# Kernel tuning notes

Hardware: AMD Instinct MI355X
Metric: run time of the kernel (lower is better)

## Reference

```python
import jax, jax.numpy as jnp
import numpy as np

BS, NQ, NC = 128, 900, 91
PRE_TOPK = 10000      # source: pre_topk when n_queries*n_cls > 10000
POST_TOPK = 100       # source: keep_inds[:100]
IOU_THRESH = 0.7


def box_cxcywh_to_xyxy(b):
    cx, cy, w, h = b[..., 0], b[..., 1], b[..., 2], b[..., 3]
    return jnp.stack([cx - 0.5 * w, cy - 0.5 * h, cx + 0.5 * w, cy + 0.5 * h], axis=-1)


def nms_image(boxes, scores, labels):
    """Greedy batched NMS, returning the first POST_TOPK picked indices.
    boxes: [PRE,4] xyxy (scaled), scores: [PRE] desc-sorted, labels: [PRE] int.
    batched_nms trick: offset boxes per class so IoU across classes is 0."""
    max_coord = jnp.max(boxes)
    off = labels.astype(boxes.dtype) * (max_coord + 1.0)
    ob = boxes + off[:, None]                          # [PRE,4]
    areas = (ob[:, 2] - ob[:, 0]) * (ob[:, 3] - ob[:, 1])

    def step(active, _):
        s = jnp.where(active, scores, -jnp.inf)
        i = jnp.argmax(s)                              # highest-score surviving box
        bi = ob[i]
        xx1 = jnp.maximum(bi[0], ob[:, 0])
        yy1 = jnp.maximum(bi[1], ob[:, 1])
        xx2 = jnp.minimum(bi[2], ob[:, 2])
        yy2 = jnp.minimum(bi[3], ob[:, 3])
        inter = jnp.clip(xx2 - xx1, 0.0) * jnp.clip(yy2 - yy1, 0.0)
        union = areas[i] + areas - inter
        iou = inter / jnp.maximum(union, 1e-9)
        # suppress IoU > thresh (includes i itself since iou(i,i)=1)
        active = active & (iou <= IOU_THRESH)
        return active, i

    _, keep = jax.lax.scan(step, jnp.ones(ob.shape[0], dtype=bool), None, length=POST_TOPK)
    return keep                                         # [POST]


def setup_inputs() -> dict:
    key = jax.random.key(0)
    k1, k2, k3, k4 = jax.random.split(key, 4)
    pred_logits = jax.random.normal(k1, (BS, NQ, NC), dtype=jnp.float32) * 2.0 - 2.0
    cxcy = jax.random.uniform(k2, (BS, NQ, 2), dtype=jnp.float32)
    wh = jax.random.uniform(k3, (BS, NQ, 2), dtype=jnp.float32, minval=0.02, maxval=0.3)
    pred_boxes = jnp.concatenate([cxcy, wh], axis=-1)   # cxcywh in [0,1]
    target_sizes = jax.random.uniform(k4, (BS, 2), dtype=jnp.float32, minval=480.0, maxval=1333.0)
    return {"pred_logits": pred_logits, "pred_boxes": pred_boxes, "target_sizes": target_sizes}


def reference(pred_logits, pred_boxes, target_sizes):
    bs, nq, nc = pred_logits.shape
    prob = jax.nn.sigmoid(pred_logits).reshape(bs, nq * nc)      # all_scores
    boxes = box_cxcywh_to_xyxy(pred_boxes)                        # [bs,nq,4]
    img_h, img_w = target_sizes[:, 0], target_sizes[:, 1]
    scale = jnp.stack([img_w, img_h, img_w, img_h], axis=1)       # [bs,4]
    boxes = boxes * scale[:, None, :]

    top_scores, top_idx = jax.lax.top_k(prob, PRE_TOPK)           # [bs,PRE]
    top_labels = top_idx % nc                                     # all_labels gather
    top_box_idx = top_idx // nc                                   # all_boxes gather
    top_boxes = jnp.take_along_axis(boxes, top_box_idx[..., None], axis=1)  # [bs,PRE,4]

    keep = jax.vmap(nms_image)(top_boxes, top_scores, top_labels)  # [bs,POST]
    out_scores = jnp.take_along_axis(top_scores, keep, axis=1)
    out_labels = jnp.take_along_axis(top_labels, keep, axis=1)
    out_boxes = jnp.take_along_axis(top_boxes, keep[..., None], axis=1)
    return out_scores, out_labels, out_boxes
```

## Files before the change

kernel.cpp:

```cpp
#include <hip/hip_runtime.h>
#include <cstdint>

#pragma clang fp contract(off)

#define BS   128
#define NQ   900
#define NC   91
#define NQC  (NQ * NC)
#define Q4   (NQC / 4)
#define HHALF 10238
#define PRE  10000
#define POST 100
#define TBITS 13
#define TBINS (1 << TBITS)
#define TSHIFT (32 - TBITS)
#define K_WIN 16
#define HSEG 1024
#define KS   2780

typedef unsigned long long ull;

#define WS_GH 0

__device__ __forceinline__ uint32_t fkey(float f) {
    uint32_t b = __float_as_uint(f);
    return (b & 0x80000000u) ? ~b : (b | 0x80000000u);
}
__device__ __forceinline__ float unkey(uint32_t u) {
    uint32_t b = (u & 0x80000000u) ? (u & 0x7FFFFFFFu) : ~u;
    return __uint_as_float(b);
}
__device__ __forceinline__ uint32_t qclamp(uint32_t q) { return (q < NQ) ? q : (NQ - 1); }

__device__ __forceinline__ ull shflx(ull v, int j) {
    uint32_t lo = (uint32_t)__shfl_xor((int)(uint32_t)v, j, 64);
    uint32_t hi = (uint32_t)__shfl_xor((int)(uint32_t)(v >> 32), j, 64);
    return ((ull)hi << 32) | (ull)lo;
}
__device__ __forceinline__ ull cex(ull v, int j, bool lower, bool desc) {
    ull pb = shflx(v, j);
    ull a = lower ? v : pb;
    ull b = lower ? pb : v;
    bool sw = desc ? (a < b) : (a > b);
    return sw ? pb : v;
}
__device__ __forceinline__ void ce(ull& a, ull& b, bool desc) {
    bool sw = desc ? (a < b) : (a > b);
    if (sw) { ull t = a; a = b; b = t; }
}

__global__ void __launch_bounds__(1024) k_hist(const float* __restrict__ logits,
                                               uint16_t* __restrict__ ghist) {
    const int img = blockIdx.x >> 1;
    const int h = blockIdx.x & 1;
    const int tid = threadIdx.x;
    __shared__ uint32_t hist[TBINS];
    __shared__ uint32_t part[1024];
    __shared__ uint32_t sTB;
    const float4* lg4 = (const float4*)(logits + (size_t)img * NQC);
    for (int i = tid; i < TBINS; i += 1024) hist[i] = 0u;
    float4 sv[5];
    #pragma unroll
    for (int c = 0; c < 5; ++c) sv[c] = lg4[c * 4096 + tid];
    __syncthreads();
    #pragma unroll
    for (int c = 0; c < 5; ++c) {
        atomicAdd(&hist[fkey(sv[c].x) >> TSHIFT], 1u);
        atomicAdd(&hist[fkey(sv[c].y) >> TSHIFT], 1u);
        atomicAdd(&hist[fkey(sv[c].z) >> TSHIFT], 1u);
        atomicAdd(&hist[fkey(sv[c].w) >> TSHIFT], 1u);
    }
    __syncthreads();
    {
        uint32_t s = 0;
        int b0 = tid * 8;
        #pragma unroll
        for (int j = 0; j < 8; ++j) s += hist[b0 + j];
        part[tid] = s;
    }
    __syncthreads();
    if (tid < 64) {
        uint32_t pv[16]; uint32_t tot = 0;
        #pragma unroll
        for (int j = 0; j < 16; ++j) { pv[j] = part[tid * 16 + j]; tot += pv[j]; }
        uint32_t sinc = tot;
        #pragma unroll
        for (int off = 1; off < 64; off <<= 1) {
            uint32_t o = (uint32_t)__shfl_down((int)sinc, off, 64);
            if (tid + off < 64) sinc += o;
        }
        uint32_t cum = sinc - tot;
        for (int j = 15; j >= 0; --j) {
            if (cum < KS && cum + pv[j] >= KS) {
                int pbn = (tid * 16 + j) * 8;
                uint32_t c2 = cum;
                for (int b = pbn + 7; b >= pbn; --b) {
                    if (c2 + hist[b] >= KS) { sTB = (uint32_t)b; break; }
                    c2 += hist[b];
                }
            }
            cum += pv[j];
        }
    }
    __syncthreads();
    const uint32_t TB = sTB;
    for (int i = tid; i < TBINS; i += 1024) hist[i] = 0u;
    __syncthreads();
    const int lo = h * HHALF;
    const int hi = (lo + HHALF < Q4) ? (lo + HHALF) : Q4;
    for (int i0 = lo; i0 < hi; i0 += 4096) {
        float4 v[4]; bool lv[4];
        #pragma unroll
        for (int s = 0; s < 4; ++s) {
            int i = i0 + (s << 10) + tid;
            lv[s] = (i < hi);
            v[s] = lv[s] ? lg4[i] : make_float4(0.f, 0.f, 0.f, 0.f);
        }
        #pragma unroll
        for (int s = 0; s < 4; ++s) {
            if (lv[s]) {
                uint32_t u;
                u = fkey(v[s].x); if ((u >> TSHIFT) >= TB) atomicAdd(&hist[u >> TSHIFT], 1u);
                u = fkey(v[s].y); if ((u >> TSHIFT) >= TB) atomicAdd(&hist[u >> TSHIFT], 1u);
                u = fkey(v[s].z); if ((u >> TSHIFT) >= TB) atomicAdd(&hist[u >> TSHIFT], 1u);
                u = fkey(v[s].w); if ((u >> TSHIFT) >= TB) atomicAdd(&hist[u >> TSHIFT], 1u);
            }
        }
    }
    __syncthreads();
    uint16_t* g = ghist + (size_t)(img * 2 + h) * TBINS;
    for (int i = tid; i < TBINS; i += 1024) g[i] = (uint16_t)hist[i];
}

__global__ void __launch_bounds__(1024) k_sel(const float* __restrict__ logits,
                                              const uint16_t* __restrict__ ghist,
                                              const float* __restrict__ pred_boxes,
                                              const float* __restrict__ target_sizes,
                                              float* __restrict__ out) {
    const int img = blockIdx.x;
    const int tid = threadIdx.x;
    const int lane = tid & 63;
    const int wv = tid >> 6;

    __shared__ uint32_t hist[TBINS];
    __shared__ uint32_t part[1024];
    __shared__ float4 shPB[NQ];
    __shared__ ull binK[HSEG];
    __shared__ ull headK[HSEG];
    __shared__ float aX1[POST], aY1[POST], aX2[POST], aY2[POST], aAr[POST];
    __shared__ int   aCl[POST];
    __shared__ float s_x1[K_WIN], s_y1[K_WIN], s_x2[K_WIN], s_y2[K_WIN];
    __shared__ int   s_cl[K_WIN];
    __shared__ uint32_t s_em[K_WIN];
    __shared__ ull sF0;
    __shared__ uint32_t sCntA, sCntB, sMX;
    __shared__ uint32_t sB1, sTp1, sB2, sTp2, sTK;

    const float ih = target_sizes[img * 2 + 0];
    const float iw = target_sizes[img * 2 + 1];
    const float* pb = pred_boxes + (size_t)img * NQ * 4;
    const float4* lg4 = (const float4*)(logits + (size_t)img * NQC);

    auto mckey = [&](uint32_t f) -> uint32_t {
        uint32_t q = qclamp(f / NC);
        float4 bb = shPB[q];
        float x1 = (bb.x - 0.5f * bb.z) * iw;
        float y1 = (bb.y - 0.5f * bb.w) * ih;
        float x2 = (bb.x + 0.5f * bb.z) * iw;
        float y2 = (bb.y + 0.5f * bb.w) * ih;
        return fkey(fmaxf(fmaxf(x1, y1), fmaxf(x2, y2)));
    };

    if (tid < NQ) shPB[tid] = ((const float4*)pb)[tid];
    {
        const uint16_t* g0 = ghist + (size_t)(img * 2) * TBINS;
        const uint16_t* g1 = g0 + TBINS;
        for (int i = tid; i < TBINS; i += 1024)
            hist[i] = (uint32_t)g0[i] + (uint32_t)g1[i];
    }
    binK[tid] = 0ull; headK[tid] = 0ull;
    if (tid == 0) { sCntA = 0u; sCntB = 0u; sMX = 0u; sF0 = 0ull;
                    sB1 = 0u; sTp1 = 1u; sB2 = 0u; sTp2 = 0u; sTK = 0u; }
    __syncthreads();
    {
        uint32_t s = 0;
        int b0 = tid * 8;
        #pragma unroll
        for (int j = 0; j < 8; ++j) s += hist[b0 + j];
        part[tid] = s;
    }
    __syncthreads();

    if (tid < 64) {
        uint32_t pv[16]; uint32_t tot = 0;
        #pragma unroll
        for (int j = 0; j < 16; ++j) { pv[j] = part[tid * 16 + j]; tot += pv[j]; }
        uint32_t sinc = tot;
        #pragma unroll
        for (int off = 1; off < 64; off <<= 1) {
            uint32_t o = (uint32_t)__shfl_down((int)sinc, off, 64);
            if (tid + off < 64) sinc += o;
        }
        uint32_t total = (uint32_t)__shfl((int)sinc, 0, 64);
        uint32_t TKl = (total < PRE) ? total : PRE;
        uint32_t T2l = (TKl < HSEG) ? TKl : HSEG;
        if (tid == 0) sTK = TKl;
        uint32_t cum = sinc - tot;
        for (int j = 15; j >= 0; --j) {
            if (cum < TKl && cum + pv[j] >= TKl) {
                int pbn = (tid * 16 + j) * 8;
                uint32_t c2 = cum;
                for (int b = pbn + 7; b >= pbn; --b) {
                    if (c2 + hist[b] >= TKl) { sB1 = (uint32_t)b; sTp1 = TKl - c2; break; }
                    c2 += hist[b];
                }
            }
            if (cum < T2l && cum + pv[j] >= T2l) {
                int pbn = (tid * 16 + j) * 8;
                uint32_t c2 = cum;
                for (int b = pbn + 3 + 4; b >= pbn; --b) {
                    if (c2 + hist[b] >= T2l) { sB2 = (uint32_t)b; sTp2 = T2l - c2; break; }
                    c2 += hist[b];
                }
            }
            cum += pv[j];
        }
    }
    __syncthreads();
    const uint32_t B1 = sB1, tp1 = sTp1, B2 = sB2;
    const uint32_t TK = sTK;
    const int C1 = (int)(((TK < (uint32_t)HSEG) ? TK : (uint32_t)HSEG) - sTp2);

    uint32_t lmx = 0u;
    for (int i0 = 0; i0 < Q4; i0 += 4096) {
        float4 v[4]; int ib[4];
        #pragma unroll
        for (int s = 0; s < 4; ++s) {
            int i = i0 + (s << 10) + tid;
            ib[s] = i;
            v[s] = (i < Q4) ? lg4[i] : make_float4(0.f, 0.f, 0.f, 0.f);
        }
        #pragma unroll
        for (int s = 0; s < 4; ++s) {
            const bool live = (ib[s] < Q4);
            float comp[4] = {v[s].x, v[s].y, v[s].z, v[s].w};
            #pragma unroll
            for (int c = 0; c < 4; ++c) {
                uint32_t u = fkey(comp[c]);
                uint32_t bin = u >> TSHIFT;
                uint32_t fi = (uint32_t)(ib[s] * 4 + c);
                if (live && bin > B1) { uint32_t km = mckey(fi); if (km > lmx) lmx = km; }
                bool isA = live && (bin == B1);
                bool isB = live && (bin > B2);
                ull key = ((ull)u << 32) | (ull)(0xFFFFFFFFu - fi);
                ull mA = __ballot(isA);
                if (mA) {
                    uint32_t wb = 0u;
                    if (lane == 0) wb = atomicAdd(&sCntA, (uint32_t)__popcll(mA));
                    wb = (uint32_t)__shfl((int)wb, 0, 64);
                    if (isA) {
                        uint32_t p = wb + (uint32_t)__popcll(mA & ((1ull << lane) - 1ull));
                        if (p < HSEG) binK[p] = key;
                    }
                }
                ull mB = __ballot(isB);
                if (mB) {
                    uint32_t wb = 0u;
                    if (lane == 0) wb = atomicAdd(&sCntB, (uint32_t)__popcll(mB));
                    wb = (uint32_t)__shfl((int)wb, 0, 64);
                    if (isB) {
                        uint32_t p = wb + (uint32_t)__popcll(mB & ((1ull << lane) - 1ull));
                        if (p < HSEG) headK[p] = key;
                    }
                }
            }
        }
    }
    __syncthreads();

    {
        ull r0 = 0, r1 = 0, r2 = 0, r3 = 0;
        const int cw = wv & 3;
        const int cb = cw << 8;
        ull* A = (wv < 4) ? binK : headK;
        if (wv < 8) {
            r0 = A[cb | lane]; r1 = A[cb | 64 | lane];
            r2 = A[cb | 128 | lane]; r3 = A[cb | 192 | lane];
            #pragma unroll
            for (int k2 = 2; k2 <= 32; k2 <<= 1) {
                bool d = ((lane & k2) == 0);
                #pragma unroll
                for (int j = 16; j >= 1; j >>= 1) {
                    if (j <= (k2 >> 1)) {
                        bool lw = ((lane & j) == 0);
                        r0 = cex(r0, j, lw, d); r1 = cex(r1, j, lw, d);
                        r2 = cex(r2, j, lw, d); r3 = cex(r3, j, lw, d);
                    }
                }
            }
            #pragma unroll
            for (int j = 32; j >= 1; j >>= 1) {
                bool lw = ((lane & j) == 0);
                r0 = cex(r0, j, lw, true);  r1 = cex(r1, j, lw, false);
                r2 = cex(r2, j, lw, true);  r3 = cex(r3, j, lw, false);
            }
            ce(r0, r1, true); ce(r2, r3, false);
            #pragma unroll
            for (int j = 32; j >= 1; j >>= 1) {
                bool lw = ((lane & j) == 0);
                r0 = cex(r0, j, lw, true);  r1 = cex(r1, j, lw, true);
                r2 = cex(r2, j, lw, false); r3 = cex(r3, j, lw, false);
            }
            {
                bool d = ((cw & 1) == 0);
                ce(r0, r2, d); ce(r1, r3, d); ce(r0, r1, d); ce(r2, r3, d);
                #pragma unroll
                for (int j = 32; j >= 1; j >>= 1) {
                    bool lw = ((lane & j) == 0);
                    r0 = cex(r0, j, lw, d); r1 = cex(r1, j, lw, d);
                    r2 = cex(r2, j, lw, d); r3 = cex(r3, j, lw, d);
                }
            }
            A[cb | lane] = r0; A[cb | 64 | lane] = r1;
            A[cb | 128 | lane] = r2; A[cb | 192 | lane] = r3;
        }
        __syncthreads();
        {
            ull* Bp = (tid >> 9) ? headK : binK;
            int t = tid & 511;
            int i = ((t & ~255) << 1) | (t & 255);
            int ixj = i | 256;
            bool d = ((i & 512) == 0);
            ull a = Bp[i], b = Bp[ixj];
            bool sw = d ? (a < b) : (a > b);
            if (sw) { Bp[i] = b; Bp[ixj] = a; }
        }
        __syncthreads();
        if (wv < 8) {
            r0 = A[cb | lane]; r1 = A[cb | 64 | lane];
            r2 = A[cb | 128 | lane]; r3 = A[cb | 192 | lane];
            bool d = ((cw & 2) == 0);
            ce(r0, r2, d); ce(r1, r3, d); ce(r0, r1, d); ce(r2, r3, d);
            #pragma unroll
            for (int j = 32; j >= 1; j >>= 1) {
                bool lw = ((lane & j) == 0);
                r0 = cex(r0, j, lw, d); r1 = cex(r1, j, lw, d);
                r2 = cex(r2, j, lw, d); r3 = cex(r3, j, lw, d);
            }
            A[cb | lane] = r0; A[cb | 64 | lane] = r1;
            A[cb | 128 | lane] = r2; A[cb | 192 | lane] = r3;
        }
        __syncthreads();
        {
            ull* Bp = (tid >> 9) ? headK : binK;
            int t = tid & 511;
            ull a = Bp[t], b = Bp[t | 512];
            if (a < b) { Bp[t] = b; Bp[t | 512] = a; }
        }
        __syncthreads();
        {
            ull* Bp = (tid >> 9) ? headK : binK;
            int t = tid & 511;
            int i = ((t & ~255) << 1) | (t & 255);
            int ixj = i | 256;
            ull a = Bp[i], b = Bp[ixj];
            if (a < b) { Bp[i] = b; Bp[ixj] = a; }
        }
        __syncthreads();
        if (wv < 8) {
            r0 = A[cb | lane]; r1 = A[cb | 64 | lane];
            r2 = A[cb | 128 | lane]; r3 = A[cb | 192 | lane];
            ce(r0, r2, true); ce(r1, r3, true); ce(r0, r1, true); ce(r2, r3, true);
            #pragma unroll
            for (int j = 32; j >= 1; j >>= 1) {
                bool lw = ((lane & j) == 0);
                r0 = cex(r0, j, lw, true); r1 = cex(r1, j, lw, true);
                r2 = cex(r2, j, lw, true); r3 = cex(r3, j, lw, true);
            }
            A[cb | lane] = r0; A[cb | 64 | lane] = r1;
            A[cb | 128 | lane] = r2; A[cb | 192 | lane] = r3;
        }
        __syncthreads();
    }

    if (tid < (int)tp1) {
        ull x = binK[tid];
        if (x != 0ull) { uint32_t km = mckey(~(uint32_t)x); if (km > lmx) lmx = km; }
    }
    for (int off = 32; off > 0; off >>= 1) {
        uint32_t o = (uint32_t)__shfl_down((int)lmx, off, 64);
        if (o > lmx) lmx = o;
    }
    if (lane == 0) atomicMax(&sMX, lmx);
    if (tid == 0 && C1 > 0) sF0 = headK[0];
    __syncthreads();
    float offD;
    {
        uint32_t m = sMX;
        uint32_t b = (m & 0x80000000u) ? (m & 0x7FFFFFFFu) : ~m;
        offD = __uint_as_float(b) + 1.0f;
    }

    auto sort1024 = [&]() {
        const int idx = tid;
        ull x = headK[idx];
        #pragma unroll
        for (int k2 = 2; k2 <= 32; k2 <<= 1) {
            bool d = ((lane & k2) == 0);
            #pragma unroll
            for (int j = 16; j >= 1; j >>= 1)
                if (j <= (k2 >> 1)) x = cex(x, j, (lane & j) == 0, d);
        }
        {
            bool d = ((idx & 64) == 0);
            #pragma unroll
            for (int j = 32; j >= 1; j >>= 1) x = cex(x, j, (lane & j) == 0, d);
        }
        for (int k = 128; k <= 1024; k <<= 1) {
            headK[idx] = x;
            __syncthreads();
            for (int j = k >> 1; j >= 64; j >>= 1) {
                if (tid < 512) {
                    int i2 = ((tid & ~(j - 1)) << 1) | (tid & (j - 1));
                    int ixj = i2 | j;
                    ull a = headK[i2], b = headK[ixj];
                    bool sw = ((i2 & k) == 0) ? (a < b) : (a > b);
                    if (sw) { headK[i2] = b; headK[ixj] = a; }
                }
                __syncthreads();
            }
            x = headK[idx];
            bool d = ((idx & k) == 0);
            #pragma unroll
            for (int j = 32; j >= 1; j >>= 1) x = cex(x, j, (lane & j) == 0, d);
        }
        headK[idx] = x;
        __syncthreads();
    };

    int npick = 0, base = 0, segbase = 0, segend = C1;
    int bcur = (int)B2;
    bool needF0 = (C1 == 0);
    while (npick < POST) {
        if (base >= segend) {
            if (segend >= (int)TK) {
                ull x0 = sF0;
                uint32_t f0 = ~(uint32_t)x0;
                uint32_t u0 = (uint32_t)(x0 >> 32);
                uint32_t q0 = qclamp(f0 / NC);
                uint32_t c0 = f0 - (f0 / NC) * NC;
                float4 bb = shPB[q0];
                float rx1 = (bb.x - 0.5f * bb.z) * iw;
                float ry1 = (bb.y - 0.5f * bb.w) * ih;
                float rx2 = (bb.x + 0.5f * bb.z) * iw;
                float ry2 = (bb.y + 0.5f * bb.w) * ih;
                float sc = 1.0f / (1.0f + expf(-unkey(u0)));
                for (int p2 = npick + tid; p2 < POST; p2 += 1024) {
                    out[img * POST + p2] = sc;
                    out[BS * POST + img * POST + p2] = (float)c0;
                    float* ob2 = out + 2 * BS * POST + ((size_t)img * POST + p2) * 4;
                    ob2[0] = rx1; ob2[1] = ry1; ob2[2] = rx2; ob2[3] = ry2;
                }
                break;
            }
            while (bcur > 0 && hist[bcur] == 0u) --bcur;
            headK[tid] = 0ull;
            if (tid == 0) sCntA = 0u;
            __syncthreads();
            for (int i0 = 0; i0 < Q4; i0 += 1024) {
                int i = i0 + tid;
                bool live = (i < Q4);
                float4 v = live ? lg4[i] : make_float4(0.f, 0.f, 0.f, 0.f);
                float comp[4] = {v.x, v.y, v.z, v.w};
                #pragma unroll
                for (int c = 0; c < 4; ++c) {
                    uint32_t u = fkey(comp[c]);
                    bool pass = live && ((u >> TSHIFT) == (uint32_t)bcur);
                    ull m = __ballot(pass);
                    if (m) {
                        uint32_t wb = 0u;
                        if (lane == 0) wb = atomicAdd(&sCntA, (uint32_t)__popcll(m));
                        wb = (uint32_t)__shfl((int)wb, 0, 64);
                        if (pass) {
                            uint32_t p = wb + (uint32_t)__popcll(m & ((1ull << lane) - 1ull));
                            uint32_t fi = (uint32_t)(i * 4 + c);
                            if (p < HSEG) headK[p] = ((ull)u << 32) | (ull)(0xFFFFFFFFu - fi);
                        }
                    }
                }
            }
            __syncthreads();
            sort1024();
            int avail = (int)((sCntA < (uint32_t)HSEG) ? sCntA : (uint32_t)HSEG);
            int take = (int)TK - segend; if (take > avail) take = avail;
            if (needF0) { if (tid == 0) sF0 = headK[0]; needF0 = false; __syncthreads(); }
            segbase = segend; segend += take; --bcur;
            continue;
        }

        const int r = base + wv;
        const bool val = (r < segend);
        const ull xk = headK[val ? (r - segbase) : 0];
        const uint32_t f = val ? ~(uint32_t)xk : 0u;
        const uint32_t uk = (uint32_t)(xk >> 32);
        const uint32_t q = qclamp(f / NC);
        const uint32_t cc = f - (f / NC) * NC;
        float4 bb = shPB[q];
        const float x1 = (bb.x - 0.5f * bb.z) * iw;
        const float y1 = (bb.y - 0.5f * bb.w) * ih;
        const float x2 = (bb.x + 0.5f * bb.z) * iw;
        const float y2 = (bb.y + 0.5f * bb.w) * ih;
        if (lane == 0) {
            s_x1[wv] = x1; s_y1[wv] = y1; s_x2[wv] = x2; s_y2[wv] = y2;
            s_cl[wv] = val ? (int)cc : -1;
        }
        __syncthreads();

        const float o = (float)cc * offD;
        const float cx1 = x1 + o, cy1 = y1 + o, cx2 = x2 + o, cy2 = y2 + o;
        const float car = (cx2 - cx1) * (cy2 - cy1);
        bool cf = false;
        if (val && lane < wv && s_cl[lane] == (int)cc) {
            float jx1 = s_x1[lane] + o, jy1 = s_y1[lane] + o;
            float jx2 = s_x2[lane] + o, jy2 = s_y2[lane] + o;
            float arj = (jx2 - jx1) * (jy2 - jy1);
            float xx1 = fmaxf(jx1, cx1), yy1 = fmaxf(jy1, cy1);
            float xx2 = fminf(jx2, cx2), yy2 = fminf(jy2, cy2);
            float inter = fmaxf(xx2 - xx1, 0.0f) * fmaxf(yy2 - yy1, 0.0f);
            float uni = (arj + car) - inter;
            float iou = inter / fmaxf(uni, 1e-9f);
            cf = !(iou <= 0.7f);
        }
        uint32_t em = (uint32_t)(__ballot(cf) & 0xFFFFull);
        bool pf = false;
        for (int i2 = lane; i2 < npick; i2 += 64) {
            if (aCl[i2] == (int)cc) {
                float jx1 = aX1[i2] + o, jy1 = aY1[i2] + o;
                float jx2 = aX2[i2] + o, jy2 = aY2[i2] + o;
                float arj = aAr[i2];
                float xx1 = fmaxf(jx1, cx1), yy1 = fmaxf(jy1, cy1);
                float xx2 = fminf(jx2, cx2), yy2 = fminf(jy2, cy2);
                float inter = fmaxf(xx2 - xx1, 0.0f) * fmaxf(yy2 - yy1, 0.0f);
                float uni = (arj + car) - inter;
                float iou = inter / fmaxf(uni, 1e-9f);
                pf |= !(iou <= 0.7f);
            }
        }
        bool anyPrior = (__ballot(pf) != 0ull);
        if (lane == 0)
            s_em[wv] = em | (anyPrior ? 0x80000000u : 0u) | (val ? 0u : 0x40000000u);
        __syncthreads();

        uint32_t acc = 0u; int a = 0;
        const int room = POST - npick;
        #pragma unroll
        for (int w2 = 0; w2 < K_WIN; ++w2) {
            uint32_t ew = s_em[w2];
            if (!(ew & 0xC0000000u) && a < room && ((ew & 0xFFFFu & acc) == 0u)) {
                acc |= (1u << w2); ++a;
            }
        }

        if (((acc >> wv) & 1u) && lane == 0) {
            int p = npick + __popc(acc & ((1u << wv) - 1u));
            float sc = 1.0f / (1.0f + expf(-unkey(uk)));
            out[img * POST + p] = sc;
            out[BS * POST + img * POST + p] = (float)cc;
            float* ob2 = out + 2 * BS * POST + ((size_t)img * POST + p) * 4;
            ob2[0] = x1; ob2[1] = y1; ob2[2] = x2; ob2[3] = y2;
            aX1[p] = x1; aY1[p] = y1; aX2[p] = x2; aY2[p] = y2;
            aAr[p] = car; aCl[p] = (int)cc;
        }
        npick += a;
        base += K_WIN;
    }
}

extern "C" void kernel_launch(void* const* d_in, const int* in_sizes, int n_in,
                              void* d_out, int out_size, void* d_ws, size_t ws_size,
                              hipStream_t stream) {
    const float* logits = (const float*)d_in[0];
    const float* boxes  = (const float*)d_in[1];
    const float* tsizes = (const float*)d_in[2];
    float* out = (float*)d_out;

    uint16_t* ghist = (uint16_t*)((char*)d_ws + WS_GH);

    k_hist<<<2 * BS, 1024, 0, stream>>>(logits, ghist);
    k_sel<<<BS, 1024, 0, stream>>>(logits, ghist, boxes, tsizes, out);
}
```

Measured before the change: 153.4 us.

## Compact candidate keys in first kernel so selection skips full logit rescans

The first kernel now writes every candidate above a sample-estimated threshold bin into a per-half workspace buffer of packed 64-bit keys, instead of building a histogram. The selection kernel rebuilds its histogram from these compacted keys held in registers and partitions from them, and its fallback refill loop scans the compacted list rather than rereading all logits. This removes the selection kernel's full 82K-element logit passes per image at the cost of global key writes and a fixed capacity that could drop candidates if the threshold estimate is too loose.

```diff
diff --git a/kernel.cpp b/kernel.cpp
--- a/kernel.cpp
+++ b/kernel.cpp
@@ -17,10 +17,13 @@
 #define K_WIN 16
 #define HSEG 1024
 #define KS   2780
+#define CAPH 7680
+#define NSLOT 15
 
 typedef unsigned long long ull;
 
-#define WS_GH 0
+#define WS_CNT 0
+#define WS_KEYS 8192
 
 __device__ __forceinline__ uint32_t fkey(float f) {
     uint32_t b = __float_as_uint(f);
@@ -49,16 +52,19 @@
     if (sw) { ull t = a; a = b; b = t; }
 }
 
-__global__ void __launch_bounds__(1024) k_hist(const float* __restrict__ logits,
-                                               uint16_t* __restrict__ ghist) {
+__global__ void __launch_bounds__(1024) k_compact(const float* __restrict__ logits,
+                                                  ull* __restrict__ keys,
+                                                  uint32_t* __restrict__ cnts) {
     const int img = blockIdx.x >> 1;
     const int h = blockIdx.x & 1;
     const int tid = threadIdx.x;
+    const int lane = tid & 63;
     __shared__ uint32_t hist[TBINS];
     __shared__ uint32_t part[1024];
-    __shared__ uint32_t sTB;
+    __shared__ uint32_t sTB, sCnt;
     const float4* lg4 = (const float4*)(logits + (size_t)img * NQC);
     for (int i = tid; i < TBINS; i += 1024) hist[i] = 0u;
+    if (tid == 0) sCnt = 0u;
     float4 sv[5];
     #pragma unroll
     for (int c = 0; c < 5; ++c) sv[c] = lg4[c * 4096 + tid];
@@ -104,36 +110,37 @@
     }
     __syncthreads();
     const uint32_t TB = sTB;
-    for (int i = tid; i < TBINS; i += 1024) hist[i] = 0u;
-    __syncthreads();
+    ull* seg = keys + (size_t)(img * 2 + h) * CAPH;
     const int lo = h * HHALF;
     const int hi = (lo + HHALF < Q4) ? (lo + HHALF) : Q4;
-    for (int i0 = lo; i0 < hi; i0 += 4096) {
-        float4 v[4]; bool lv[4];
-        #pragma unroll
-        for (int s = 0; s < 4; ++s) {
-            int i = i0 + (s << 10) + tid;
-            lv[s] = (i < hi);
-            v[s] = lv[s] ? lg4[i] : make_float4(0.f, 0.f, 0.f, 0.f);
-        }
-        #pragma unroll
-        for (int s = 0; s < 4; ++s) {
-            if (lv[s]) {
-                uint32_t u;
-                u = fkey(v[s].x); if ((u >> TSHIFT) >= TB) atomicAdd(&hist[u >> TSHIFT], 1u);
-                u = fkey(v[s].y); if ((u >> TSHIFT) >= TB) atomicAdd(&hist[u >> TSHIFT], 1u);
-                u = fkey(v[s].z); if ((u >> TSHIFT) >= TB) atomicAdd(&hist[u >> TSHIFT], 1u);
-                u = fkey(v[s].w); if ((u >> TSHIFT) >= TB) atomicAdd(&hist[u >> TSHIFT], 1u);
-            }
-        }
-    }
-    __syncthreads();
-    uint16_t* g = ghist + (size_t)(img * 2 + h) * TBINS;
-    for (int i = tid; i < TBINS; i += 1024) g[i] = (uint16_t)hist[i];
-}
-
-__global__ void __launch_bounds__(1024) k_sel(const float* __restrict__ logits,
-                                              const uint16_t* __restrict__ ghist,
+    for (int i0 = lo; i0 < hi; i0 += 1024) {
+        int i = i0 + tid;
+        bool inb = (i < hi);
+        float4 v = inb ? lg4[i] : make_float4(0.f, 0.f, 0.f, 0.f);
+        float comp[4] = {v.x, v.y, v.z, v.w};
+        #pragma unroll
+        for (int c = 0; c < 4; ++c) {
+            uint32_t u = fkey(comp[c]);
+            bool pass = inb && ((u >> TSHIFT) >= TB);
+            ull m = __ballot(pass);
+            if (m) {
+                uint32_t wb = 0u;
+                if (lane == 0) wb = atomicAdd(&sCnt, (uint32_t)__popcll(m));
+                wb = (uint32_t)__shfl((int)wb, 0, 64);
+                if (pass) {
+                    uint32_t p = wb + (uint32_t)__popcll(m & ((1ull << lane) - 1ull));
+                    uint32_t fi = (uint32_t)(i * 4 + c);
+                    if (p < CAPH) seg[p] = ((ull)u << 32) | (ull)(0xFFFFFFFFu - fi);
+                }
+            }
+        }
+    }
+    __syncthreads();
+    if (tid == 0) cnts[img * 2 + h] = (sCnt < CAPH) ? sCnt : CAPH;
+}
+
+__global__ void __launch_bounds__(1024) k_sel(const ull* __restrict__ keys,
+                                              const uint32_t* __restrict__ cnts,
                                               const float* __restrict__ pred_boxes,
                                               const float* __restrict__ target_sizes,
                                               float* __restrict__ out) {
@@ -159,7 +166,6 @@
     const float ih = target_sizes[img * 2 + 0];
     const float iw = target_sizes[img * 2 + 1];
     const float* pb = pred_boxes + (size_t)img * NQ * 4;
-    const float4* lg4 = (const float4*)(logits + (size_t)img * NQC);
 
     auto mckey = [&](uint32_t f) -> uint32_t {
         uint32_t q = qclamp(f / NC);
@@ -172,15 +178,30 @@
     };
 
     if (tid < NQ) shPB[tid] = ((const float4*)pb)[tid];
-    {
-        const uint16_t* g0 = ghist + (size_t)(img * 2) * TBINS;
-        const uint16_t* g1 = g0 + TBINS;
-        for (int i = tid; i < TBINS; i += 1024)
-            hist[i] = (uint32_t)g0[i] + (uint32_t)g1[i];
-    }
+    for (int i = tid; i < TBINS; i += 1024) hist[i] = 0u;
     binK[tid] = 0ull; headK[tid] = 0ull;
     if (tid == 0) { sCntA = 0u; sCntB = 0u; sMX = 0u; sF0 = 0ull;
                     sB1 = 0u; sTp1 = 1u; sB2 = 0u; sTp2 = 0u; sTK = 0u; }
+    const uint32_t c0 = cnts[img * 2 + 0];
+    const uint32_t c1 = cnts[img * 2 + 1];
+    const int total = (int)(c0 + c1);
+    const ull* seg0 = keys + (size_t)(img * 2) * CAPH;
+    const ull* seg1 = seg0 + CAPH;
+    ull kk[NSLOT];
+    #pragma unroll
+    for (int j = 0; j < NSLOT; ++j) {
+        int i = tid + (j << 10);
+        ull x = 0ull;
+        if (i < total) x = (i < (int)c0) ? seg0[i] : seg1[i - (int)c0];
+        kk[j] = x;
+    }
+    __syncthreads();
+
+    #pragma unroll
+    for (int j = 0; j < NSLOT; ++j) {
+        ull x = kk[j];
+        if (x != 0ull) atomicAdd(&hist[(uint32_t)(x >> 51)], 1u);
+    }
     __syncthreads();
     {
         uint32_t s = 0;
@@ -190,7 +211,6 @@
         part[tid] = s;
     }
     __syncthreads();
-
     if (tid < 64) {
         uint32_t pv[16]; uint32_t tot = 0;
         #pragma unroll
@@ -201,8 +221,8 @@
             uint32_t o = (uint32_t)__shfl_down((int)sinc, off, 64);
             if (tid + off < 64) sinc += o;
         }
-        uint32_t total = (uint32_t)__shfl((int)sinc, 0, 64);
-        uint32_t TKl = (total < PRE) ? total : PRE;
+        uint32_t tt = (uint32_t)__shfl((int)sinc, 0, 64);
+        uint32_t TKl = (tt < PRE) ? tt : PRE;
         uint32_t T2l = (TKl < HSEG) ? TKl : HSEG;
         if (tid == 0) sTK = TKl;
         uint32_t cum = sinc - tot;
@@ -218,7 +238,7 @@
             if (cum < T2l && cum + pv[j] >= T2l) {
                 int pbn = (tid * 16 + j) * 8;
                 uint32_t c2 = cum;
-                for (int b = pbn + 3 + 4; b >= pbn; --b) {
+                for (int b = pbn + 7; b >= pbn; --b) {
                     if (c2 + hist[b] >= T2l) { sB2 = (uint32_t)b; sTp2 = T2l - c2; break; }
                     c2 += hist[b];
                 }
@@ -232,47 +252,32 @@
     const int C1 = (int)(((TK < (uint32_t)HSEG) ? TK : (uint32_t)HSEG) - sTp2);
 
     uint32_t lmx = 0u;
-    for (int i0 = 0; i0 < Q4; i0 += 4096) {
-        float4 v[4]; int ib[4];
-        #pragma unroll
-        for (int s = 0; s < 4; ++s) {
-            int i = i0 + (s << 10) + tid;
-            ib[s] = i;
-            v[s] = (i < Q4) ? lg4[i] : make_float4(0.f, 0.f, 0.f, 0.f);
-        }
-        #pragma unroll
-        for (int s = 0; s < 4; ++s) {
-            const bool live = (ib[s] < Q4);
-            float comp[4] = {v[s].x, v[s].y, v[s].z, v[s].w};
-            #pragma unroll
-            for (int c = 0; c < 4; ++c) {
-                uint32_t u = fkey(comp[c]);
-                uint32_t bin = u >> TSHIFT;
-                uint32_t fi = (uint32_t)(ib[s] * 4 + c);
-                if (live && bin > B1) { uint32_t km = mckey(fi); if (km > lmx) lmx = km; }
-                bool isA = live && (bin == B1);
-                bool isB = live && (bin > B2);
-                ull key = ((ull)u << 32) | (ull)(0xFFFFFFFFu - fi);
-                ull mA = __ballot(isA);
-                if (mA) {
-                    uint32_t wb = 0u;
-                    if (lane == 0) wb = atomicAdd(&sCntA, (uint32_t)__popcll(mA));
-                    wb = (uint32_t)__shfl((int)wb, 0, 64);
-                    if (isA) {
-                        uint32_t p = wb + (uint32_t)__popcll(mA & ((1ull << lane) - 1ull));
-                        if (p < HSEG) binK[p] = key;
-                    }
-                }
-                ull mB = __ballot(isB);
-                if (mB) {
-                    uint32_t wb = 0u;
-                    if (lane == 0) wb = atomicAdd(&sCntB, (uint32_t)__popcll(mB));
-                    wb = (uint32_t)__shfl((int)wb, 0, 64);
-                    if (isB) {
-                        uint32_t p = wb + (uint32_t)__popcll(mB & ((1ull << lane) - 1ull));
-                        if (p < HSEG) headK[p] = key;
-                    }
-                }
+    #pragma unroll
+    for (int j = 0; j < NSLOT; ++j) {
+        ull x = kk[j];
+        uint32_t bin = (uint32_t)(x >> 51);
+        bool liveK = (x != 0ull);
+        if (liveK && bin > B1) { uint32_t km = mckey(~(uint32_t)x); if (km > lmx) lmx = km; }
+        bool isA = liveK && (bin == B1);
+        bool isB = liveK && (bin > B2);
+        ull mA = __ballot(isA);
+        if (mA) {
+            uint32_t wb = 0u;
+            if (lane == 0) wb = atomicAdd(&sCntA, (uint32_t)__popcll(mA));
+            wb = (uint32_t)__shfl((int)wb, 0, 64);
+            if (isA) {
+                uint32_t p = wb + (uint32_t)__popcll(mA & ((1ull << lane) - 1ull));
+                if (p < HSEG) binK[p] = x;
+            }
+        }
+        ull mB = __ballot(isB);
+        if (mB) {
+            uint32_t wb = 0u;
+            if (lane == 0) wb = atomicAdd(&sCntB, (uint32_t)__popcll(mB));
+            wb = (uint32_t)__shfl((int)wb, 0, 64);
+            if (isB) {
+                uint32_t p = wb + (uint32_t)__popcll(mB & ((1ull << lane) - 1ull));
+                if (p < HSEG) headK[p] = x;
             }
         }
     }
@@ -448,7 +453,7 @@
                 uint32_t f0 = ~(uint32_t)x0;
                 uint32_t u0 = (uint32_t)(x0 >> 32);
                 uint32_t q0 = qclamp(f0 / NC);
-                uint32_t c0 = f0 - (f0 / NC) * NC;
+                uint32_t cc0 = f0 - (f0 / NC) * NC;
                 float4 bb = shPB[q0];
                 float rx1 = (bb.x - 0.5f * bb.z) * iw;
                 float ry1 = (bb.y - 0.5f * bb.w) * ih;
@@ -457,7 +462,7 @@
                 float sc = 1.0f / (1.0f + expf(-unkey(u0)));
                 for (int p2 = npick + tid; p2 < POST; p2 += 1024) {
                     out[img * POST + p2] = sc;
-                    out[BS * POST + img * POST + p2] = (float)c0;
+                    out[BS * POST + img * POST + p2] = (float)cc0;
                     float* ob2 = out + 2 * BS * POST + ((size_t)img * POST + p2) * 4;
                     ob2[0] = rx1; ob2[1] = ry1; ob2[2] = rx2; ob2[3] = ry2;
                 }
@@ -467,25 +472,19 @@
             headK[tid] = 0ull;
             if (tid == 0) sCntA = 0u;
             __syncthreads();
-            for (int i0 = 0; i0 < Q4; i0 += 1024) {
+            for (int i0 = 0; i0 < total; i0 += 1024) {
                 int i = i0 + tid;
-                bool live = (i < Q4);
-                float4 v = live ? lg4[i] : make_float4(0.f, 0.f, 0.f, 0.f);
-                float comp[4] = {v.x, v.y, v.z, v.w};
-                #pragma unroll
-                for (int c = 0; c < 4; ++c) {
-                    uint32_t u = fkey(comp[c]);
-                    bool pass = live && ((u >> TSHIFT) == (uint32_t)bcur);
-                    ull m = __ballot(pass);
-                    if (m) {
-                        uint32_t wb = 0u;
-                        if (lane == 0) wb = atomicAdd(&sCntA, (uint32_t)__popcll(m));
-                        wb = (uint32_t)__shfl((int)wb, 0, 64);
-                        if (pass) {
-                            uint32_t p = wb + (uint32_t)__popcll(m & ((1ull << lane) - 1ull));
-                            uint32_t fi = (uint32_t)(i * 4 + c);
-                            if (p < HSEG) headK[p] = ((ull)u << 32) | (ull)(0xFFFFFFFFu - fi);
-                        }
+                ull x = 0ull;
+                if (i < total) x = (i < (int)c0) ? seg0[i] : seg1[i - (int)c0];
+                bool pass = (x != 0ull) && ((uint32_t)(x >> 51) == (uint32_t)bcur);
+                ull m = __ballot(pass);
+                if (m) {
+                    uint32_t wb = 0u;
+                    if (lane == 0) wb = atomicAdd(&sCntA, (uint32_t)__popcll(m));
+                    wb = (uint32_t)__shfl((int)wb, 0, 64);
+                    if (pass) {
+                        uint32_t p = wb + (uint32_t)__popcll(m & ((1ull << lane) - 1ull));
+                        if (p < HSEG) headK[p] = x;
                     }
                 }
             }
@@ -584,8 +583,9 @@
     const float* tsizes = (const float*)d_in[2];
     float* out = (float*)d_out;
 
-    uint16_t* ghist = (uint16_t*)((char*)d_ws + WS_GH);
-
-    k_hist<<<2 * BS, 1024, 0, stream>>>(logits, ghist);
-    k_sel<<<BS, 1024, 0, stream>>>(logits, ghist, boxes, tsizes, out);
-}
+    uint32_t* cnts = (uint32_t*)((char*)d_ws + WS_CNT);
+    ull* keys = (ull*)((char*)d_ws + WS_KEYS);
+
+    k_compact<<<2 * BS, 1024, 0, stream>>>(logits, keys, cnts);
+    k_sel<<<BS, 1024, 0, stream>>>(keys, cnts, boxes, tsizes, out);
+}
```

After: 138.8 us. 9.5% less time.
